# Kernel tuning notes

Measured on AMD Instinct MI355X. Metric: run time of the kernel, lower is better.

## Reference

```python
import jax, jax.numpy as jnp
import numpy as np

# ---- Clifford algebra Cl(3,0): 8 blades ordered by grade: [1, e1,e2,e3, e12,e13,e23, e123] ----
_ORDER = [0, 1, 2, 4, 3, 5, 6, 7]  # bitmask of each blade in grade-sorted order
GRADES = np.array([0, 1, 1, 1, 2, 2, 2, 3])  # grade (subspace) of each blade
EPS = 1e-6

def _build_cayley():
    C = np.zeros((8, 8, 8), np.float32)
    for ia, a in enumerate(_ORDER):
        for ib, b in enumerate(_ORDER):
            # reordering sign from anticommuting basis vectors (Euclidean metric -> squares +1)
            t, tot = a >> 1, 0
            while t:
                tot += bin(t & b).count("1")
                t >>= 1
            s = 1.0 if tot % 2 == 0 else -1.0
            C[ia, ib, _ORDER.index(a ^ b)] = s
    return jnp.asarray(C)

CAYLEY = _build_cayley()  # [8,8,8], highly sparse (64 nonzeros)

def mvlinear(x, W, b):
    # x: [B,N,Cin,8], W: [Cout,Cin,4] per-grade weights, b: [Cout] bias on scalar blade
    Wf = W[:, :, GRADES]                               # [Cout,Cin,8] via repeat over grades [1,3,3,1]
    y = jnp.einsum("bnci,oci->bnoi", x, Wf)
    return y.at[..., 0].add(b)

def setup_inputs() -> dict:
    key = jax.random.key(0)
    ks = jax.random.split(key, 5)
    B, N, Cin, Ch = 8, 4096, 64, 128
    return {
        "x": jax.random.normal(ks[0], (B, N, Cin, 8), jnp.float32),
        "W1": jax.random.normal(ks[1], (Ch, Cin, 4), jnp.float32) / np.sqrt(Cin),
        "b1": jax.random.normal(ks[2], (Ch,), jnp.float32) * 0.02,
        "W2": jax.random.normal(ks[3], (Cin, Ch, 4), jnp.float32) / np.sqrt(Ch),
        "b2": jax.random.normal(ks[4], (Cin,), jnp.float32) * 0.02,
        "a": jnp.ones((Cin,), jnp.float32),
    }

def reference(x, W1, b1, W2, b2, a):
    h = mvlinear(x, W1, b1)                                   # [B,N,Ch,8]
    h = jnp.einsum("bnci,ijk,bncj->bnck", h, CAYLEY, h)       # geometric product (sparse Cayley)
    y = mvlinear(h, W2, b2)                                   # [B,N,Cin,8]
    # MVLayerNorm: per-channel multivector norm (Euclidean: sqrt(sum of squares)),
    # averaged over channels, then scale by learned a
    norm = jnp.sqrt(jnp.sum(y * y, axis=-1, keepdims=True))   # [B,N,Cin,1]
    denom = jnp.mean(norm, axis=-2, keepdims=True) + EPS      # [B,N,1,1]
    return a[None, None, :, None] * y / denom
```

## Files before the change

### kernel.cpp

```cpp
#include <hip/hip_runtime.h>
#include <stdint.h>

typedef unsigned short u16;
typedef __attribute__((ext_vector_type(4))) float f32x4;
typedef __attribute__((ext_vector_type(8))) __bf16 bf16x8;

struct Cay { int idx[8][8]; float sgn[8][8]; };
constexpr int kOrder[8] = {0,1,2,4,3,5,6,7};
constexpr int ordpos(int m){ int r=-1; for(int i=0;i<8;i++) if(kOrder[i]==m) r=i; return r; }
constexpr Cay make_cay(){
  Cay c{};
  for(int ia=0; ia<8; ia++) for(int ib=0; ib<8; ib++){
    int a=kOrder[ia], b=kOrder[ib];
    int t=a>>1, tot=0;
    while(t){ int x=t&b; while(x){ tot+=x&1; x>>=1; } t>>=1; }
    c.idx[ia][ib]=ordpos(a^b);
    c.sgn[ia][ib]=(tot&1)?-1.0f:1.0f;
  }
  return c;
}
constexpr Cay CAY = make_cay();

struct GPTab { float dsgn[8]; int np; int pi[28]; int pj[28]; int pk[28]; float ps[28]; };
constexpr GPTab make_gptab(){
  GPTab t{};
  for (int i=0;i<8;i++) t.dsgn[i] = CAY.sgn[i][i];
  t.np = 0;
  for (int i=0;i<8;i++) for (int j=i+1;j<8;j++){
    float s = CAY.sgn[i][j] + CAY.sgn[j][i];
    if (s != 0.0f){ t.pi[t.np]=i; t.pj[t.np]=j; t.pk[t.np]=CAY.idx[i][j];
                    t.ps[t.np]=(s>0.f)?1.0f:-1.0f; t.np++; }
  }
  return t;
}
constexpr GPTab GPT = make_gptab();

__device__ __forceinline__ void gprod_half(const float* h, float* g){
  float g0 = h[0]*h[0];
  #pragma unroll
  for (int i=1;i<8;i++) g0 = fmaf(GPT.dsgn[i]>0.f ? h[i] : -h[i], h[i], g0);
  g[0] = g0;
  #pragma unroll
  for (int k=1;k<8;k++) g[k] = 0.f;
  #pragma unroll
  for (int t=0;t<GPT.np;t++)
    g[GPT.pk[t]] = fmaf(GPT.ps[t]>0.f ? h[GPT.pi[t]] : -h[GPT.pi[t]],
                        h[GPT.pj[t]], g[GPT.pk[t]]);
}

__device__ __forceinline__ u16 f2bf(float f){
  union { float f; uint32_t u; } v; v.f=f;
  uint32_t u=v.u;
  return (u16)((u + 0x7fffu + ((u>>16)&1u)) >> 16);
}

__device__ __forceinline__ uint32_t cvtpk(float lo, float hi){
  uint32_t r;
  asm("v_cvt_pk_bf16_f32 %0, %1, %2" : "=v"(r) : "v"(lo), "v"(hi));
  return r;
}

__global__ void gp_prepack(const float* __restrict__ W1, const float* __restrict__ W2,
                           u16* __restrict__ w1p, u16* __restrict__ w2p)
{
  int t = blockIdx.x*256 + threadIdx.x;
  int e = t & 7, l = (t>>3)&63, f = t>>9;
  int lm = l & 15, lh = l >> 4;
  if (f < 64) {
    int g = f >> 4, ks = (f>>3)&1, ot = f&7;
    int o = ot*16 + lm, c = ks*32 + lh*8 + e;
    w1p[f*512 + l*8 + e] = f2bf(W1[(o*64 + c)*4 + g]);
  } else {
    int f2 = f - 64;
    int g = f2 >> 4, ks = (f2>>2)&3, ot = f2&3;
    int outc = ot*16 + lm, o = ks*32 + lh*8 + e;
    float sc = (g == 0) ? 1.0f : 2.0f;
    w2p[f2*512 + l*8 + e] = f2bf(W2[(outc*128 + o)*4 + g] * sc);
  }
}

__global__ __launch_bounds__(256,5) void gp_fused(
    const float* __restrict__ x, const u16* __restrict__ w1p,
    const float* __restrict__ b1, const u16* __restrict__ w2p,
    const float* __restrict__ b2, const float* __restrict__ avec,
    float* __restrict__ out)
{
  __shared__ __align__(16) char SH[32768];
  float* redArr = reinterpret_cast<float*>(SH);

  const int tid = threadIdx.x;
  const int w  = tid >> 6;
  const int l  = tid & 63;
  const int lm = l & 15;
  const int lh = l >> 4;
  const int xk = (lm & 7) << 4;

  {
    const int cp = tid & 31;
    const int pr = tid >> 5;
    const float4* xt = reinterpret_cast<const float4*>(x) + (size_t)blockIdx.x * 2048;
    #pragma unroll
    for (int it=0; it<2; ++it){
      const int p = pr + it*8;
      const float4* src = xt + p*128 + cp*4;
      float4 v0 = src[0], v1 = src[1], v2 = src[2], v3 = src[3];
      uint32_t pk[8];
      pk[0]=cvtpk(v0.x,v2.x); pk[1]=cvtpk(v0.y,v2.y); pk[2]=cvtpk(v0.z,v2.z); pk[3]=cvtpk(v0.w,v2.w);
      pk[4]=cvtpk(v1.x,v3.x); pk[5]=cvtpk(v1.y,v3.y); pk[6]=cvtpk(v1.z,v3.z); pk[7]=cvtpk(v1.w,v3.w);
      const int xo = (p & 7) << 4;
      #pragma unroll
      for (int b=0;b<8;b++)
        *reinterpret_cast<uint32_t*>(SH + ((((p*8+b)<<7) + (cp<<2)) ^ xo)) = pk[b];
    }
  }
  __syncthreads();

  constexpr int BSTART[4] = {0,1,4,7};
  constexpr int BCNT[4]   = {1,3,3,1};

  f32x4 acc1[2][8];
  #pragma unroll
  for (int cc=0; cc<2; ++cc)
    #pragma unroll
    for (int b=0; b<8; ++b)
      acc1[cc][b] = (f32x4){0.f,0.f,0.f,0.f};

  const uint4* w1f = reinterpret_cast<const uint4*>(w1p);
  #pragma unroll
  for (int g4=0; g4<4; ++g4){
    #pragma unroll
    for (int ks=0; ks<2; ++ks){
      uint4 wa = w1f[((g4*2+ks)*8 + w    )*64 + l];
      uint4 wb = w1f[((g4*2+ks)*8 + w + 4)*64 + l];
      bf16x8 wav = __builtin_bit_cast(bf16x8, wa);
      bf16x8 wbv = __builtin_bit_cast(bf16x8, wb);
      #pragma unroll
      for (int bi=0; bi<3; ++bi){
        if (bi >= BCNT[g4]) break;
        const int blade = BSTART[g4] + bi;
        bf16x8 xv = *reinterpret_cast<const bf16x8*>(
            SH + ((((lm*8+blade)<<7) + ((ks*32+lh*8)<<1)) ^ xk));
        acc1[0][blade] = __builtin_amdgcn_mfma_f32_16x16x32_bf16(wav, xv, acc1[0][blade], 0,0,0);
        acc1[1][blade] = __builtin_amdgcn_mfma_f32_16x16x32_bf16(wbv, xv, acc1[1][blade], 0,0,0);
      }
    }
  }
  __syncthreads();

  #pragma unroll
  for (int cc=0; cc<2; ++cc){
    const int cht = w + cc*4;
    const float4 b14 = reinterpret_cast<const float4*>(b1)[cht*4 + lh];
    const float bb[4] = {b14.x, b14.y, b14.z, b14.w};
    uint32_t lo[8], hi[8];
    #pragma unroll
    for (int rp=0; rp<2; ++rp){
      float ga[8], gb[8];
      {
        float h[8];
        #pragma unroll
        for (int b=0;b<8;b++) h[b] = acc1[cc][b][rp*2+0];
        h[0] += bb[rp*2+0];
        gprod_half(h, ga);
      }
      {
        float h[8];
        #pragma unroll
        for (int b=0;b<8;b++) h[b] = acc1[cc][b][rp*2+1];
        h[0] += bb[rp*2+1];
        gprod_half(h, gb);
      }
      #pragma unroll
      for (int b=0;b<8;b++){
        uint32_t v = cvtpk(ga[b], gb[b]);
        if (rp==0) lo[b] = v; else hi[b] = v;
      }
    }
    const int chByte = (cht*16 + lh*4) << 1;
    #pragma unroll
    for (int b=0;b<8;b++){
      uint2 v; v.x = lo[b]; v.y = hi[b];
      *reinterpret_cast<uint2*>(SH + ((((lm*8+b)<<8) + chByte) ^ xk)) = v;
    }
  }
  __syncthreads();

  f32x4 acc2[8];
  #pragma unroll
  for (int b=0; b<8; ++b) acc2[b] = (f32x4){0.f,0.f,0.f,0.f};

  const uint4* w2f = reinterpret_cast<const uint4*>(w2p);
  #pragma unroll
  for (int ks=0; ks<4; ++ks){
    #pragma unroll
    for (int g4=0; g4<4; ++g4){
      uint4 wu = w2f[((g4*4+ks)*4 + w)*64 + l];
      bf16x8 wv = __builtin_bit_cast(bf16x8, wu);
      #pragma unroll
      for (int bi=0; bi<3; ++bi){
        if (bi >= BCNT[g4]) break;
        const int blade = BSTART[g4] + bi;
        bf16x8 gv = *reinterpret_cast<const bf16x8*>(
            SH + ((((lm*8+blade)<<8) + ((ks*32+lh*8)<<1)) ^ xk));
        acc2[blade] = __builtin_amdgcn_mfma_f32_16x16x32_bf16(gv, wv, acc2[blade], 0,0,0);
      }
    }
  }

  const int oc = w*16 + lm;
  const float b2v  = b2[oc];
  const float aval = avec[oc];
  #pragma unroll
  for (int r=0; r<4; ++r) acc2[0][r] += b2v;

  float nrm[4];
  #pragma unroll
  for (int r=0; r<4; ++r) {
    float s = 0.f;
    #pragma unroll
    for (int b=0; b<8; ++b) s = fmaf(acc2[b][r], acc2[b][r], s);
    nrm[r] = sqrtf(s);
  }
  #pragma unroll
  for (int r=0; r<4; ++r) {
    float v = nrm[r];
    v += __shfl_xor(v, 1, 64);
    v += __shfl_xor(v, 2, 64);
    v += __shfl_xor(v, 4, 64);
    v += __shfl_xor(v, 8, 64);
    nrm[r] = v;
  }
  __syncthreads();
  if (lm == 0) {
    #pragma unroll
    for (int r=0; r<4; ++r) redArr[(lh*4 + r)*4 + w] = nrm[r];
  }
  __syncthreads();

  #pragma unroll
  for (int r=0; r<4; ++r) {
    const int pos = lh*4 + r;
    const float4 rr = *reinterpret_cast<const float4*>(redArr + pos*4);
    const float denom = (rr.x+rr.y+rr.z+rr.w) * (1.0f/64.0f) + 1e-6f;
    const float sc = aval / denom;
    float4 o0, o1;
    o0.x = acc2[0][r]*sc; o0.y = acc2[1][r]*sc; o0.z = acc2[2][r]*sc; o0.w = acc2[3][r]*sc;
    o1.x = acc2[4][r]*sc; o1.y = acc2[5][r]*sc; o1.z = acc2[6][r]*sc; o1.w = acc2[7][r]*sc;
    size_t P = (size_t)blockIdx.x*16 + pos;
    float4* op = reinterpret_cast<float4*>(out + (P*64 + (size_t)oc)*8);
    op[0] = o0; op[1] = o1;
  }
}

extern "C" void kernel_launch(void* const* d_in, const int* in_sizes, int n_in,
                              void* d_out, int out_size, void* d_ws, size_t ws_size,
                              hipStream_t stream)
{
  const float* x  = (const float*)d_in[0];
  const float* W1 = (const float*)d_in[1];
  const float* b1 = (const float*)d_in[2];
  const float* W2 = (const float*)d_in[3];
  const float* b2 = (const float*)d_in[4];
  const float* a  = (const float*)d_in[5];
  float* out = (float*)d_out;

  u16* w1p = (u16*)d_ws;
  u16* w2p = w1p + 32768;

  gp_prepack<<<256, 256, 0, stream>>>(W1, W2, w1p, w2p);
  gp_fused<<<2048, 256, 0, stream>>>(x, w1p, b1, w2p, b2, a, out);
}
```

Baseline: 45.81 us.

## Load x directly into MFMA register fragments, skipping LDS staging

Each lane now loads its own x slice from global memory straight into registers and packs it into bf16 MFMA B-fragments, so the shared-memory write, the barrier and the LDS reads for the first GEMM are gone. The first GEMM is also restructured to run one channel tile at a time, computing the geometric product right after each tile's MFMAs, which roughly halves the live accumulator registers. Occupancy is lowered from 5 to 4 waves per SIMD to make room for the 32 float4 staging registers. The risk is less coalesced global loads (each lane reads 256 contiguous bytes) and higher register pressure.

```diff
diff --git a/kernel.cpp b/kernel.cpp
--- a/kernel.cpp
+++ b/kernel.cpp
@@ -58,6 +58,10 @@
   uint32_t r;
   asm("v_cvt_pk_bf16_f32 %0, %1, %2" : "=v"(r) : "v"(lo), "v"(hi));
   return r;
+}
+
+__device__ __forceinline__ float fc(const float4& v, int c){
+  switch(c){ case 0: return v.x; case 1: return v.y; case 2: return v.z; default: return v.w; }
 }
 
 __global__ void gp_prepack(const float* __restrict__ W1, const float* __restrict__ W2,
@@ -79,7 +83,7 @@
   }
 }
 
-__global__ __launch_bounds__(256,5) void gp_fused(
+__global__ __launch_bounds__(256,4) void gp_fused(
     const float* __restrict__ x, const u16* __restrict__ w1p,
     const float* __restrict__ b1, const u16* __restrict__ w2p,
     const float* __restrict__ b2, const float* __restrict__ avec,
@@ -95,61 +99,55 @@
   const int lh = l >> 4;
   const int xk = (lm & 7) << 4;
 
-  {
-    const int cp = tid & 31;
-    const int pr = tid >> 5;
-    const float4* xt = reinterpret_cast<const float4*>(x) + (size_t)blockIdx.x * 2048;
-    #pragma unroll
-    for (int it=0; it<2; ++it){
-      const int p = pr + it*8;
-      const float4* src = xt + p*128 + cp*4;
-      float4 v0 = src[0], v1 = src[1], v2 = src[2], v3 = src[3];
-      uint32_t pk[8];
-      pk[0]=cvtpk(v0.x,v2.x); pk[1]=cvtpk(v0.y,v2.y); pk[2]=cvtpk(v0.z,v2.z); pk[3]=cvtpk(v0.w,v2.w);
-      pk[4]=cvtpk(v1.x,v3.x); pk[5]=cvtpk(v1.y,v3.y); pk[6]=cvtpk(v1.z,v3.z); pk[7]=cvtpk(v1.w,v3.w);
-      const int xo = (p & 7) << 4;
-      #pragma unroll
-      for (int b=0;b<8;b++)
-        *reinterpret_cast<uint32_t*>(SH + ((((p*8+b)<<7) + (cp<<2)) ^ xo)) = pk[b];
-    }
-  }
-  __syncthreads();
-
   constexpr int BSTART[4] = {0,1,4,7};
   constexpr int BCNT[4]   = {1,3,3,1};
 
-  f32x4 acc1[2][8];
-  #pragma unroll
-  for (int cc=0; cc<2; ++cc)
-    #pragma unroll
-    for (int b=0; b<8; ++b)
-      acc1[cc][b] = (f32x4){0.f,0.f,0.f,0.f};
+  const float4* px = reinterpret_cast<const float4*>(x)
+                   + ((size_t)blockIdx.x*16 + lm)*128 + lh*16;
+  float4 va[16], vb[16];
+  #pragma unroll
+  for (int i=0;i<16;++i) va[i] = px[i];
+  #pragma unroll
+  for (int i=0;i<16;++i) vb[i] = px[64+i];
+
+  uint4 frg[2][8];
+  #pragma unroll
+  for (int b=0; b<8; ++b){
+    const int hb = b >> 2, c = b & 3;
+    frg[0][b].x = cvtpk(fc(va[0+hb],c),  fc(va[2+hb],c));
+    frg[0][b].y = cvtpk(fc(va[4+hb],c),  fc(va[6+hb],c));
+    frg[0][b].z = cvtpk(fc(va[8+hb],c),  fc(va[10+hb],c));
+    frg[0][b].w = cvtpk(fc(va[12+hb],c), fc(va[14+hb],c));
+    frg[1][b].x = cvtpk(fc(vb[0+hb],c),  fc(vb[2+hb],c));
+    frg[1][b].y = cvtpk(fc(vb[4+hb],c),  fc(vb[6+hb],c));
+    frg[1][b].z = cvtpk(fc(vb[8+hb],c),  fc(vb[10+hb],c));
+    frg[1][b].w = cvtpk(fc(vb[12+hb],c), fc(vb[14+hb],c));
+  }
 
   const uint4* w1f = reinterpret_cast<const uint4*>(w1p);
-  #pragma unroll
-  for (int g4=0; g4<4; ++g4){
-    #pragma unroll
-    for (int ks=0; ks<2; ++ks){
-      uint4 wa = w1f[((g4*2+ks)*8 + w    )*64 + l];
-      uint4 wb = w1f[((g4*2+ks)*8 + w + 4)*64 + l];
-      bf16x8 wav = __builtin_bit_cast(bf16x8, wa);
-      bf16x8 wbv = __builtin_bit_cast(bf16x8, wb);
-      #pragma unroll
-      for (int bi=0; bi<3; ++bi){
-        if (bi >= BCNT[g4]) break;
-        const int blade = BSTART[g4] + bi;
-        bf16x8 xv = *reinterpret_cast<const bf16x8*>(
-            SH + ((((lm*8+blade)<<7) + ((ks*32+lh*8)<<1)) ^ xk));
-        acc1[0][blade] = __builtin_amdgcn_mfma_f32_16x16x32_bf16(wav, xv, acc1[0][blade], 0,0,0);
-        acc1[1][blade] = __builtin_amdgcn_mfma_f32_16x16x32_bf16(wbv, xv, acc1[1][blade], 0,0,0);
-      }
-    }
-  }
-  __syncthreads();
-
   #pragma unroll
   for (int cc=0; cc<2; ++cc){
     const int cht = w + cc*4;
+    f32x4 acc1[8];
+    #pragma unroll
+    for (int b=0; b<8; ++b) acc1[b] = (f32x4){0.f,0.f,0.f,0.f};
+
+    #pragma unroll
+    for (int g4=0; g4<4; ++g4){
+      #pragma unroll
+      for (int ks=0; ks<2; ++ks){
+        uint4 wu = w1f[((g4*2+ks)*8 + cht)*64 + l];
+        bf16x8 wv = __builtin_bit_cast(bf16x8, wu);
+        #pragma unroll
+        for (int bi=0; bi<3; ++bi){
+          if (bi >= BCNT[g4]) break;
+          const int blade = BSTART[g4] + bi;
+          bf16x8 xv = __builtin_bit_cast(bf16x8, frg[ks][blade]);
+          acc1[blade] = __builtin_amdgcn_mfma_f32_16x16x32_bf16(wv, xv, acc1[blade], 0,0,0);
+        }
+      }
+    }
+
     const float4 b14 = reinterpret_cast<const float4*>(b1)[cht*4 + lh];
     const float bb[4] = {b14.x, b14.y, b14.z, b14.w};
     uint32_t lo[8], hi[8];
@@ -159,14 +157,14 @@
       {
         float h[8];
         #pragma unroll
-        for (int b=0;b<8;b++) h[b] = acc1[cc][b][rp*2+0];
+        for (int b=0;b<8;b++) h[b] = acc1[b][rp*2+0];
         h[0] += bb[rp*2+0];
         gprod_half(h, ga);
       }
       {
         float h[8];
         #pragma unroll
-        for (int b=0;b<8;b++) h[b] = acc1[cc][b][rp*2+1];
+        for (int b=0;b<8;b++) h[b] = acc1[b][rp*2+1];
         h[0] += bb[rp*2+1];
         gprod_half(h, gb);
       }
```

Result: slower. 60.03 us (+31.0%).

## Give each wavefront its own 16-point tile and stream hidden channels through registers

Applied to the files above, without the earlier changes.

Each wavefront now handles a full 16-point tile independently: it computes the first linear layer in hidden-channel chunks, applies the geometric product, and feeds the results straight into the second GEMM through ds_bpermute lane shuffles. The shared-memory round trip for the hidden activations, the block-wide barriers and the cross-wave norm reduction are all removed. In exchange, each wave holds 4x more accumulators and reloads W1/W2 fragments per tile. The grid shrinks to 512 blocks with 64KB of LDS at launch bounds of 2, which lowers occupancy.

```diff
diff --git a/kernel.cpp b/kernel.cpp
--- a/kernel.cpp
+++ b/kernel.cpp
@@ -79,150 +79,164 @@
   }
 }
 
-__global__ __launch_bounds__(256,5) void gp_fused(
+__global__ __launch_bounds__(256,2) void gp_fused(
     const float* __restrict__ x, const u16* __restrict__ w1p,
     const float* __restrict__ b1, const u16* __restrict__ w2p,
     const float* __restrict__ b2, const float* __restrict__ avec,
     float* __restrict__ out)
 {
-  __shared__ __align__(16) char SH[32768];
-  float* redArr = reinterpret_cast<float*>(SH);
+  __shared__ __align__(16) char SH[65536];
 
   const int tid = threadIdx.x;
   const int w  = tid >> 6;
   const int l  = tid & 63;
   const int lm = l & 15;
   const int lh = l >> 4;
-  const int xk = (lm & 7) << 4;
+  char* XSH = SH + (w << 14);
+  const size_t tile = (size_t)blockIdx.x*4 + w;
+
+  constexpr int BSTART[4] = {0,1,4,7};
+  constexpr int BCNT[4]   = {1,3,3,1};
+
+  const uint4*  w1f = reinterpret_cast<const uint4*>(w1p);
+  const uint4*  w2f = reinterpret_cast<const uint4*>(w2p);
+  const float4* b1f = reinterpret_cast<const float4*>(b1);
 
   {
-    const int cp = tid & 31;
-    const int pr = tid >> 5;
-    const float4* xt = reinterpret_cast<const float4*>(x) + (size_t)blockIdx.x * 2048;
-    #pragma unroll
-    for (int it=0; it<2; ++it){
-      const int p = pr + it*8;
+    const float4* xt = reinterpret_cast<const float4*>(x) + tile*2048;
+    #pragma unroll
+    for (int it=0; it<8; ++it){
+      const int p  = it*2 + (l>>5);
+      const int cp = l & 31;
       const float4* src = xt + p*128 + cp*4;
-      float4 v0 = src[0], v1 = src[1], v2 = src[2], v3 = src[3];
+      float4 v0=src[0], v1=src[1], v2=src[2], v3=src[3];
       uint32_t pk[8];
       pk[0]=cvtpk(v0.x,v2.x); pk[1]=cvtpk(v0.y,v2.y); pk[2]=cvtpk(v0.z,v2.z); pk[3]=cvtpk(v0.w,v2.w);
       pk[4]=cvtpk(v1.x,v3.x); pk[5]=cvtpk(v1.y,v3.y); pk[6]=cvtpk(v1.z,v3.z); pk[7]=cvtpk(v1.w,v3.w);
       const int xo = (p & 7) << 4;
       #pragma unroll
       for (int b=0;b<8;b++)
-        *reinterpret_cast<uint32_t*>(SH + ((((p*8+b)<<7) + (cp<<2)) ^ xo)) = pk[b];
-    }
-  }
-  __syncthreads();
-
-  constexpr int BSTART[4] = {0,1,4,7};
-  constexpr int BCNT[4]   = {1,3,3,1};
-
-  f32x4 acc1[2][8];
-  #pragma unroll
-  for (int cc=0; cc<2; ++cc)
-    #pragma unroll
-    for (int b=0; b<8; ++b)
-      acc1[cc][b] = (f32x4){0.f,0.f,0.f,0.f};
-
-  const uint4* w1f = reinterpret_cast<const uint4*>(w1p);
-  #pragma unroll
-  for (int g4=0; g4<4; ++g4){
-    #pragma unroll
-    for (int ks=0; ks<2; ++ks){
-      uint4 wa = w1f[((g4*2+ks)*8 + w    )*64 + l];
-      uint4 wb = w1f[((g4*2+ks)*8 + w + 4)*64 + l];
-      bf16x8 wav = __builtin_bit_cast(bf16x8, wa);
-      bf16x8 wbv = __builtin_bit_cast(bf16x8, wb);
+        *reinterpret_cast<uint32_t*>(XSH + ((((p*8+b)<<7) + (cp<<2)) ^ xo)) = pk[b];
+    }
+  }
+
+  const int xk = (lm & 7) << 4;
+  const int pa_addr0 = (lm + ((lh & 1) << 5)) << 2;
+  const int pa_addr1 = pa_addr0 + 64;
+  const bool selA = (lh < 2);
+
+  f32x4 acc2[4][8];
+  #pragma unroll
+  for (int ot=0; ot<4; ++ot)
+    #pragma unroll
+    for (int b=0; b<8; ++b) acc2[ot][b] = (f32x4){0.f,0.f,0.f,0.f};
+
+  #pragma unroll 1
+  for (int s=0; s<4; ++s){
+    uint32_t packA[16], packB[16];
+
+    #pragma unroll
+    for (int half=0; half<2; ++half){
+      const int cht = 2*s + half;
+      uint4 wf[8];
+      #pragma unroll
+      for (int i=0;i<8;++i) wf[i] = w1f[(i*8 + cht)*64 + l];
+
+      f32x4 acc1[8];
+      #pragma unroll
+      for (int b=0;b<8;++b) acc1[b] = (f32x4){0.f,0.f,0.f,0.f};
+
+      #pragma unroll
+      for (int g4=0; g4<4; ++g4){
+        #pragma unroll
+        for (int ks=0; ks<2; ++ks){
+          bf16x8 wv = __builtin_bit_cast(bf16x8, wf[g4*2+ks]);
+          #pragma unroll
+          for (int bi=0; bi<3; ++bi){
+            if (bi >= BCNT[g4]) break;
+            const int blade = BSTART[g4] + bi;
+            bf16x8 xv = *reinterpret_cast<const bf16x8*>(
+                XSH + ((((lm*8+blade)<<7) + ((ks*32+lh*8)<<1)) ^ xk));
+            acc1[blade] = __builtin_amdgcn_mfma_f32_16x16x32_bf16(wv, xv, acc1[blade], 0,0,0);
+          }
+        }
+      }
+
+      const float4 bb4 = b1f[cht*4 + lh];
+      const float bb[4] = {bb4.x, bb4.y, bb4.z, bb4.w};
+      float gg[4][8];
+      #pragma unroll
+      for (int r=0; r<4; ++r){
+        float h[8];
+        #pragma unroll
+        for (int b=0;b<8;b++) h[b] = acc1[b][r];
+        h[0] += bb[r];
+        gprod_half(h, gg[r]);
+      }
+      uint32_t* dst = half ? packB : packA;
+      #pragma unroll
+      for (int b=0;b<8;b++){
+        dst[b*2+0] = cvtpk(gg[0][b], gg[1][b]);
+        dst[b*2+1] = cvtpk(gg[2][b], gg[3][b]);
+      }
+    }
+
+    #pragma unroll
+    for (int g4=0; g4<4; ++g4){
+      uint4 wq0 = w2f[((g4*4+s)*4 + 0)*64 + l];
+      uint4 wq1 = w2f[((g4*4+s)*4 + 1)*64 + l];
+      uint4 wq2 = w2f[((g4*4+s)*4 + 2)*64 + l];
+      uint4 wq3 = w2f[((g4*4+s)*4 + 3)*64 + l];
       #pragma unroll
       for (int bi=0; bi<3; ++bi){
         if (bi >= BCNT[g4]) break;
-        const int blade = BSTART[g4] + bi;
-        bf16x8 xv = *reinterpret_cast<const bf16x8*>(
-            SH + ((((lm*8+blade)<<7) + ((ks*32+lh*8)<<1)) ^ xk));
-        acc1[0][blade] = __builtin_amdgcn_mfma_f32_16x16x32_bf16(wav, xv, acc1[0][blade], 0,0,0);
-        acc1[1][blade] = __builtin_amdgcn_mfma_f32_16x16x32_bf16(wbv, xv, acc1[1][blade], 0,0,0);
-      }
-    }
-  }
-  __syncthreads();
-
-  #pragma unroll
-  for (int cc=0; cc<2; ++cc){
-    const int cht = w + cc*4;
-    const float4 b14 = reinterpret_cast<const float4*>(b1)[cht*4 + lh];
-    const float bb[4] = {b14.x, b14.y, b14.z, b14.w};
-    uint32_t lo[8], hi[8];
-    #pragma unroll
-    for (int rp=0; rp<2; ++rp){
-      float ga[8], gb[8];
-      {
-        float h[8];
-        #pragma unroll
-        for (int b=0;b<8;b++) h[b] = acc1[cc][b][rp*2+0];
-        h[0] += bb[rp*2+0];
-        gprod_half(h, ga);
-      }
-      {
-        float h[8];
-        #pragma unroll
-        for (int b=0;b<8;b++) h[b] = acc1[cc][b][rp*2+1];
-        h[0] += bb[rp*2+1];
-        gprod_half(h, gb);
-      }
-      #pragma unroll
-      for (int b=0;b<8;b++){
-        uint32_t v = cvtpk(ga[b], gb[b]);
-        if (rp==0) lo[b] = v; else hi[b] = v;
-      }
-    }
-    const int chByte = (cht*16 + lh*4) << 1;
-    #pragma unroll
-    for (int b=0;b<8;b++){
-      uint2 v; v.x = lo[b]; v.y = hi[b];
-      *reinterpret_cast<uint2*>(SH + ((((lm*8+b)<<8) + chByte) ^ xk)) = v;
-    }
-  }
-  __syncthreads();
-
-  f32x4 acc2[8];
-  #pragma unroll
-  for (int b=0; b<8; ++b) acc2[b] = (f32x4){0.f,0.f,0.f,0.f};
-
-  const uint4* w2f = reinterpret_cast<const uint4*>(w2p);
-  #pragma unroll
-  for (int ks=0; ks<4; ++ks){
-    #pragma unroll
-    for (int g4=0; g4<4; ++g4){
-      uint4 wu = w2f[((g4*4+ks)*4 + w)*64 + l];
-      bf16x8 wv = __builtin_bit_cast(bf16x8, wu);
-      #pragma unroll
-      for (int bi=0; bi<3; ++bi){
-        if (bi >= BCNT[g4]) break;
-        const int blade = BSTART[g4] + bi;
-        bf16x8 gv = *reinterpret_cast<const bf16x8*>(
-            SH + ((((lm*8+blade)<<8) + ((ks*32+lh*8)<<1)) ^ xk));
-        acc2[blade] = __builtin_amdgcn_mfma_f32_16x16x32_bf16(gv, wv, acc2[blade], 0,0,0);
-      }
-    }
-  }
-
-  const int oc = w*16 + lm;
-  const float b2v  = b2[oc];
-  const float aval = avec[oc];
-  #pragma unroll
-  for (int r=0; r<4; ++r) acc2[0][r] += b2v;
+        const int b = BSTART[g4] + bi;
+        uint32_t tA, tB;
+        uint4 pu;
+        tA = __builtin_amdgcn_ds_bpermute(pa_addr0, packA[b*2+0]);
+        tB = __builtin_amdgcn_ds_bpermute(pa_addr0, packB[b*2+0]);
+        pu.x = selA ? tA : tB;
+        tA = __builtin_amdgcn_ds_bpermute(pa_addr0, packA[b*2+1]);
+        tB = __builtin_amdgcn_ds_bpermute(pa_addr0, packB[b*2+1]);
+        pu.y = selA ? tA : tB;
+        tA = __builtin_amdgcn_ds_bpermute(pa_addr1, packA[b*2+0]);
+        tB = __builtin_amdgcn_ds_bpermute(pa_addr1, packB[b*2+0]);
+        pu.z = selA ? tA : tB;
+        tA = __builtin_amdgcn_ds_bpermute(pa_addr1, packA[b*2+1]);
+        tB = __builtin_amdgcn_ds_bpermute(pa_addr1, packB[b*2+1]);
+        pu.w = selA ? tA : tB;
+        bf16x8 pav = __builtin_bit_cast(bf16x8, pu);
+        acc2[0][b] = __builtin_amdgcn_mfma_f32_16x16x32_bf16(pav, __builtin_bit_cast(bf16x8, wq0), acc2[0][b], 0,0,0);
+        acc2[1][b] = __builtin_amdgcn_mfma_f32_16x16x32_bf16(pav, __builtin_bit_cast(bf16x8, wq1), acc2[1][b], 0,0,0);
+        acc2[2][b] = __builtin_amdgcn_mfma_f32_16x16x32_bf16(pav, __builtin_bit_cast(bf16x8, wq2), acc2[2][b], 0,0,0);
+        acc2[3][b] = __builtin_amdgcn_mfma_f32_16x16x32_bf16(pav, __builtin_bit_cast(bf16x8, wq3), acc2[3][b], 0,0,0);
+      }
+    }
+  }
+
+  float b2v[4], av[4];
+  #pragma unroll
+  for (int ot=0; ot<4; ++ot){ b2v[ot] = b2[ot*16+lm]; av[ot] = avec[ot*16+lm]; }
+  #pragma unroll
+  for (int ot=0; ot<4; ++ot)
+    #pragma unroll
+    for (int r=0; r<4; ++r) acc2[ot][0][r] += b2v[ot];
 
   float nrm[4];
   #pragma unroll
-  for (int r=0; r<4; ++r) {
-    float s = 0.f;
-    #pragma unroll
-    for (int b=0; b<8; ++b) s = fmaf(acc2[b][r], acc2[b][r], s);
-    nrm[r] = sqrtf(s);
-  }
-  #pragma unroll
-  for (int r=0; r<4; ++r) {
+  for (int r=0; r<4; ++r){
+    float sum = 0.f;
+    #pragma unroll
+    for (int ot=0; ot<4; ++ot){
+      float ss = 0.f;
+      #pragma unroll
+      for (int b=0; b<8; ++b) ss = fmaf(acc2[ot][b][r], acc2[ot][b][r], ss);
+      sum += sqrtf(ss);
+    }
+    nrm[r] = sum;
+  }
+  #pragma unroll
+  for (int r=0; r<4; ++r){
     float v = nrm[r];
     v += __shfl_xor(v, 1, 64);
     v += __shfl_xor(v, 2, 64);
@@ -230,25 +244,23 @@
     v += __shfl_xor(v, 8, 64);
     nrm[r] = v;
   }
-  __syncthreads();
-  if (lm == 0) {
-    #pragma unroll
-    for (int r=0; r<4; ++r) redArr[(lh*4 + r)*4 + w] = nrm[r];
-  }
-  __syncthreads();
-
-  #pragma unroll
-  for (int r=0; r<4; ++r) {
-    const int pos = lh*4 + r;
-    const float4 rr = *reinterpret_cast<const float4*>(redArr + pos*4);
-    const float denom = (rr.x+rr.y+rr.z+rr.w) * (1.0f/64.0f) + 1e-6f;
-    const float sc = aval / denom;
-    float4 o0, o1;
-    o0.x = acc2[0][r]*sc; o0.y = acc2[1][r]*sc; o0.z = acc2[2][r]*sc; o0.w = acc2[3][r]*sc;
-    o1.x = acc2[4][r]*sc; o1.y = acc2[5][r]*sc; o1.z = acc2[6][r]*sc; o1.w = acc2[7][r]*sc;
-    size_t P = (size_t)blockIdx.x*16 + pos;
-    float4* op = reinterpret_cast<float4*>(out + (P*64 + (size_t)oc)*8);
-    op[0] = o0; op[1] = o1;
+
+  #pragma unroll
+  for (int r=0; r<4; ++r){
+    const float denom = nrm[r]*(1.0f/64.0f) + 1e-6f;
+    const float rde = __builtin_amdgcn_rcpf(denom);
+    const size_t P = tile*16 + (size_t)(lh*4 + r);
+    #pragma unroll
+    for (int ot=0; ot<4; ++ot){
+      const float sc = av[ot] * rde;
+      float4 o0, o1;
+      o0.x = acc2[ot][0][r]*sc; o0.y = acc2[ot][1][r]*sc;
+      o0.z = acc2[ot][2][r]*sc; o0.w = acc2[ot][3][r]*sc;
+      o1.x = acc2[ot][4][r]*sc; o1.y = acc2[ot][5][r]*sc;
+      o1.z = acc2[ot][6][r]*sc; o1.w = acc2[ot][7][r]*sc;
+      float4* op = reinterpret_cast<float4*>(out + (P*64 + (size_t)(ot*16+lm))*8);
+      op[0] = o0; op[1] = o1;
+    }
   }
 }
 
@@ -268,5 +280,5 @@
   u16* w2p = w1p + 32768;
 
   gp_prepack<<<256, 256, 0, stream>>>(W1, W2, w1p, w2p);
-  gp_fused<<<2048, 256, 0, stream>>>(x, w1p, b1, w2p, b2, a, out);
-}
+  gp_fused<<<512, 256, 0, stream>>>(x, w1p, b1, w2p, b2, a, out);
+}
```

New measurement: 53.04 us. 15.8% more time.

## Split hidden channels into two halves to cut accumulator registers, reuse x LDS region

Applied to the files above, without the earlier changes.

Computes the first linear layer and geometric product in two sequential halves of 64 hidden channels each, so only 8 accumulator tiles are live at a time instead of 16. The first half is staged in LDS and consumed by the second GEMM while the second half is kept packed in registers, then written over the x buffer and consumed. The aim is to reduce register pressure and LDS footprint per block, at the cost of extra barriers and a launch bound lowered from 5 to 4 waves. It also swaps the XOR swizzle so only the in-row offset is XORed, moves the reduction array to a separate slot so one barrier can be dropped, and uses a fast reciprocal instead of division.

```diff
diff --git a/kernel.cpp b/kernel.cpp
--- a/kernel.cpp
+++ b/kernel.cpp
@@ -79,14 +79,15 @@
   }
 }
 
-__global__ __launch_bounds__(256,5) void gp_fused(
+__global__ __launch_bounds__(256,4) void gp_fused(
     const float* __restrict__ x, const u16* __restrict__ w1p,
     const float* __restrict__ b1, const u16* __restrict__ w2p,
     const float* __restrict__ b2, const float* __restrict__ avec,
     float* __restrict__ out)
 {
-  __shared__ __align__(16) char SH[32768];
-  float* redArr = reinterpret_cast<float*>(SH);
+  __shared__ __align__(16) char SH[33024];
+  float* redArr = reinterpret_cast<float*>(SH + 32768);
+  char* G0 = SH + 16384;
 
   const int tid = threadIdx.x;
   const int w  = tid >> 6;
@@ -95,10 +96,22 @@
   const int lh = l >> 4;
   const int xk = (lm & 7) << 4;
 
+  constexpr int BSTART[4] = {0,1,4,7};
+  constexpr int BCNT[4]   = {1,3,3,1};
+
+  const float4* xb  = reinterpret_cast<const float4*>(x);
+  const uint4*  w1f = reinterpret_cast<const uint4*>(w1p);
+  const uint4*  w2f = reinterpret_cast<const uint4*>(w2p);
+  const float4* b1f = reinterpret_cast<const float4*>(b1);
+
+  const int oc = w*16 + lm;
+  const float b2v  = b2[oc];
+  const float aval = avec[oc];
+
   {
     const int cp = tid & 31;
     const int pr = tid >> 5;
-    const float4* xt = reinterpret_cast<const float4*>(x) + (size_t)blockIdx.x * 2048;
+    const float4* xt = xb + (size_t)blockIdx.x * 2048;
     #pragma unroll
     for (int it=0; it<2; ++it){
       const int p = pr + it*8;
@@ -110,88 +123,107 @@
       const int xo = (p & 7) << 4;
       #pragma unroll
       for (int b=0;b<8;b++)
-        *reinterpret_cast<uint32_t*>(SH + ((((p*8+b)<<7) + (cp<<2)) ^ xo)) = pk[b];
-    }
-  }
-  __syncthreads();
-
-  constexpr int BSTART[4] = {0,1,4,7};
-  constexpr int BCNT[4]   = {1,3,3,1};
-
-  f32x4 acc1[2][8];
-  #pragma unroll
-  for (int cc=0; cc<2; ++cc)
-    #pragma unroll
-    for (int b=0; b<8; ++b)
-      acc1[cc][b] = (f32x4){0.f,0.f,0.f,0.f};
-
-  const uint4* w1f = reinterpret_cast<const uint4*>(w1p);
-  #pragma unroll
-  for (int g4=0; g4<4; ++g4){
-    #pragma unroll
-    for (int ks=0; ks<2; ++ks){
-      uint4 wa = w1f[((g4*2+ks)*8 + w    )*64 + l];
-      uint4 wb = w1f[((g4*2+ks)*8 + w + 4)*64 + l];
-      bf16x8 wav = __builtin_bit_cast(bf16x8, wa);
-      bf16x8 wbv = __builtin_bit_cast(bf16x8, wb);
-      #pragma unroll
-      for (int bi=0; bi<3; ++bi){
-        if (bi >= BCNT[g4]) break;
-        const int blade = BSTART[g4] + bi;
-        bf16x8 xv = *reinterpret_cast<const bf16x8*>(
-            SH + ((((lm*8+blade)<<7) + ((ks*32+lh*8)<<1)) ^ xk));
-        acc1[0][blade] = __builtin_amdgcn_mfma_f32_16x16x32_bf16(wav, xv, acc1[0][blade], 0,0,0);
-        acc1[1][blade] = __builtin_amdgcn_mfma_f32_16x16x32_bf16(wbv, xv, acc1[1][blade], 0,0,0);
-      }
-    }
-  }
-  __syncthreads();
-
-  #pragma unroll
-  for (int cc=0; cc<2; ++cc){
-    const int cht = w + cc*4;
-    const float4 b14 = reinterpret_cast<const float4*>(b1)[cht*4 + lh];
+        *reinterpret_cast<uint32_t*>(SH + (((p*8+b)<<7) + ((cp<<2) ^ xo))) = pk[b];
+    }
+  }
+  __syncthreads();
+
+  {
+    f32x4 acc1[8];
+    #pragma unroll
+    for (int b=0;b<8;++b) acc1[b] = (f32x4){0.f,0.f,0.f,0.f};
+    #pragma unroll
+    for (int g4=0; g4<4; ++g4){
+      #pragma unroll
+      for (int ks=0; ks<2; ++ks){
+        uint4 wu = w1f[((g4*2+ks)*8 + w)*64 + l];
+        bf16x8 wv = __builtin_bit_cast(bf16x8, wu);
+        #pragma unroll
+        for (int bi=0; bi<3; ++bi){
+          if (bi >= BCNT[g4]) break;
+          const int blade = BSTART[g4] + bi;
+          bf16x8 xv = *reinterpret_cast<const bf16x8*>(
+              SH + (((lm*8+blade)<<7) + (((ks*32+lh*8)<<1) ^ xk)));
+          acc1[blade] = __builtin_amdgcn_mfma_f32_16x16x32_bf16(wv, xv, acc1[blade], 0,0,0);
+        }
+      }
+    }
+    const float4 b14 = b1f[w*4 + lh];
     const float bb[4] = {b14.x, b14.y, b14.z, b14.w};
-    uint32_t lo[8], hi[8];
+    uint32_t glo[8], ghi[8];
     #pragma unroll
     for (int rp=0; rp<2; ++rp){
       float ga[8], gb[8];
-      {
-        float h[8];
-        #pragma unroll
-        for (int b=0;b<8;b++) h[b] = acc1[cc][b][rp*2+0];
-        h[0] += bb[rp*2+0];
-        gprod_half(h, ga);
-      }
-      {
-        float h[8];
-        #pragma unroll
-        for (int b=0;b<8;b++) h[b] = acc1[cc][b][rp*2+1];
-        h[0] += bb[rp*2+1];
-        gprod_half(h, gb);
-      }
+      { float h[8];
+        #pragma unroll
+        for (int b=0;b<8;b++) h[b] = acc1[b][rp*2+0];
+        h[0] += bb[rp*2+0]; gprod_half(h, ga); }
+      { float h[8];
+        #pragma unroll
+        for (int b=0;b<8;b++) h[b] = acc1[b][rp*2+1];
+        h[0] += bb[rp*2+1]; gprod_half(h, gb); }
       #pragma unroll
       for (int b=0;b<8;b++){
         uint32_t v = cvtpk(ga[b], gb[b]);
-        if (rp==0) lo[b] = v; else hi[b] = v;
-      }
-    }
-    const int chByte = (cht*16 + lh*4) << 1;
+        if (rp==0) glo[b] = v; else ghi[b] = v;
+      }
+    }
+    const int chB = w*32 + lh*8;
     #pragma unroll
     for (int b=0;b<8;b++){
-      uint2 v; v.x = lo[b]; v.y = hi[b];
-      *reinterpret_cast<uint2*>(SH + ((((lm*8+b)<<8) + chByte) ^ xk)) = v;
-    }
-  }
-  __syncthreads();
+      uint2 v; v.x = glo[b]; v.y = ghi[b];
+      *reinterpret_cast<uint2*>(G0 + (((lm*8+b)<<7) + (chB ^ xk))) = v;
+    }
+  }
+  __syncthreads();
+
+  uint32_t g1lo[8], g1hi[8];
+  {
+    f32x4 acc1[8];
+    #pragma unroll
+    for (int b=0;b<8;++b) acc1[b] = (f32x4){0.f,0.f,0.f,0.f};
+    #pragma unroll
+    for (int g4=0; g4<4; ++g4){
+      #pragma unroll
+      for (int ks=0; ks<2; ++ks){
+        uint4 wu = w1f[((g4*2+ks)*8 + w + 4)*64 + l];
+        bf16x8 wv = __builtin_bit_cast(bf16x8, wu);
+        #pragma unroll
+        for (int bi=0; bi<3; ++bi){
+          if (bi >= BCNT[g4]) break;
+          const int blade = BSTART[g4] + bi;
+          bf16x8 xv = *reinterpret_cast<const bf16x8*>(
+              SH + (((lm*8+blade)<<7) + (((ks*32+lh*8)<<1) ^ xk)));
+          acc1[blade] = __builtin_amdgcn_mfma_f32_16x16x32_bf16(wv, xv, acc1[blade], 0,0,0);
+        }
+      }
+    }
+    const float4 b14 = b1f[(w+4)*4 + lh];
+    const float bb[4] = {b14.x, b14.y, b14.z, b14.w};
+    #pragma unroll
+    for (int rp=0; rp<2; ++rp){
+      float ga[8], gb[8];
+      { float h[8];
+        #pragma unroll
+        for (int b=0;b<8;b++) h[b] = acc1[b][rp*2+0];
+        h[0] += bb[rp*2+0]; gprod_half(h, ga); }
+      { float h[8];
+        #pragma unroll
+        for (int b=0;b<8;b++) h[b] = acc1[b][rp*2+1];
+        h[0] += bb[rp*2+1]; gprod_half(h, gb); }
+      #pragma unroll
+      for (int b=0;b<8;b++){
+        uint32_t v = cvtpk(ga[b], gb[b]);
+        if (rp==0) g1lo[b] = v; else g1hi[b] = v;
+      }
+    }
+  }
 
   f32x4 acc2[8];
   #pragma unroll
-  for (int b=0; b<8; ++b) acc2[b] = (f32x4){0.f,0.f,0.f,0.f};
-
-  const uint4* w2f = reinterpret_cast<const uint4*>(w2p);
-  #pragma unroll
-  for (int ks=0; ks<4; ++ks){
+  for (int b=0;b<8;++b) acc2[b] = (f32x4){0.f,0.f,0.f,0.f};
+  #pragma unroll
+  for (int ks=0; ks<2; ++ks){
     #pragma unroll
     for (int g4=0; g4<4; ++g4){
       uint4 wu = w2f[((g4*4+ks)*4 + w)*64 + l];
@@ -201,15 +233,40 @@
         if (bi >= BCNT[g4]) break;
         const int blade = BSTART[g4] + bi;
         bf16x8 gv = *reinterpret_cast<const bf16x8*>(
-            SH + ((((lm*8+blade)<<8) + ((ks*32+lh*8)<<1)) ^ xk));
+            G0 + (((lm*8+blade)<<7) + ((ks*64 + lh*16) ^ xk)));
         acc2[blade] = __builtin_amdgcn_mfma_f32_16x16x32_bf16(gv, wv, acc2[blade], 0,0,0);
       }
     }
   }
-
-  const int oc = w*16 + lm;
-  const float b2v  = b2[oc];
-  const float aval = avec[oc];
+  __syncthreads();
+
+  {
+    const int chB = w*32 + lh*8;
+    #pragma unroll
+    for (int b=0;b<8;b++){
+      uint2 v; v.x = g1lo[b]; v.y = g1hi[b];
+      *reinterpret_cast<uint2*>(SH + (((lm*8+b)<<7) + (chB ^ xk))) = v;
+    }
+  }
+  __syncthreads();
+
+  #pragma unroll
+  for (int ks=2; ks<4; ++ks){
+    #pragma unroll
+    for (int g4=0; g4<4; ++g4){
+      uint4 wu = w2f[((g4*4+ks)*4 + w)*64 + l];
+      bf16x8 wv = __builtin_bit_cast(bf16x8, wu);
+      #pragma unroll
+      for (int bi=0; bi<3; ++bi){
+        if (bi >= BCNT[g4]) break;
+        const int blade = BSTART[g4] + bi;
+        bf16x8 gv = *reinterpret_cast<const bf16x8*>(
+            SH + (((lm*8+blade)<<7) + (((ks-2)*64 + lh*16) ^ xk)));
+        acc2[blade] = __builtin_amdgcn_mfma_f32_16x16x32_bf16(gv, wv, acc2[blade], 0,0,0);
+      }
+    }
+  }
+
   #pragma unroll
   for (int r=0; r<4; ++r) acc2[0][r] += b2v;
 
@@ -230,7 +287,6 @@
     v += __shfl_xor(v, 8, 64);
     nrm[r] = v;
   }
-  __syncthreads();
   if (lm == 0) {
     #pragma unroll
     for (int r=0; r<4; ++r) redArr[(lh*4 + r)*4 + w] = nrm[r];
@@ -242,7 +298,7 @@
     const int pos = lh*4 + r;
     const float4 rr = *reinterpret_cast<const float4*>(redArr + pos*4);
     const float denom = (rr.x+rr.y+rr.z+rr.w) * (1.0f/64.0f) + 1e-6f;
-    const float sc = aval / denom;
+    const float sc = aval * __builtin_amdgcn_rcpf(denom);
     float4 o0, o1;
     o0.x = acc2[0][r]*sc; o0.y = acc2[1][r]*sc; o0.z = acc2[2][r]*sc; o0.w = acc2[3][r]*sc;
     o1.x = acc2[4][r]*sc; o1.y = acc2[5][r]*sc; o1.z = acc2[6][r]*sc; o1.w = acc2[7][r]*sc;
```

Result: no change. 44.96 us (-1.9%).
